# Kernel optimization log

Hardware: AMD Instinct MI355X
Metric: run time of the kernel (lower is better)

## Reference

```python
import jax, jax.numpy as jnp
import numpy as np
import jax.scipy.linalg as jsl

# ---- module constants (mirror __init__ buffers) ----
T0, T1, DT = 0.0, 1.0, 1e-3
DIM, NSTEPS, M, TQ, B = 8, 2048, 64, 1024, 1
DS = (T1 - T0) / NSTEPS
STEPS = jnp.linspace(T0, T1, NSTEPS + 1)            # [S+1]
ZPTS = jnp.linspace(T0 + DT * 5.5, T1 - DT * 5.5, M)  # inducing points [M]
SQRT_DS = float(np.sqrt(DS))
SQRT_DT = float(np.sqrt(DT))


def _hurst(t, y0, W1, b1, W2, b2, Wc1, bc1, Wc2, bc2, dw, cw):
    # compute_hurst: sigmoid(driving_action(t)*dw + condition_net(y0)*cw)
    tc_in = t.reshape(-1, 1)                                             # [N,1]
    feat = jnp.concatenate([jnp.sin(tc_in), jnp.cos(tc_in), tc_in], -1)  # [N,3]
    tc = jax.nn.sigmoid(jnp.tanh(feat @ W1.T + b1) @ W2.T + b2)          # [N,dim]
    pc = jax.nn.sigmoid(jnp.tanh(y0 @ Wc1.T + bc1) @ Wc2.T + bc2)        # [1,dim]
    return jax.nn.sigmoid(tc * dw + pc * cw)                             # [N,dim]


def _safe_pow(x, a):
    # x**a for x>=0, with well-defined (zero) gradient at x==0
    mask = x > 0
    xs = jnp.where(mask, x, 1.0)
    return jnp.where(mask, xs ** a, 0.0)


def _compute_weight(t, y0, params, eps=1e-12):
    # compute_weight (Muniandy et al. weight); returns [S, N, dim]
    h = _hurst(t, y0, *params)[None]                              # [1,N,dim]
    d0 = jax.nn.relu(t[None, :] - STEPS[:-1, None])[..., None]    # [S,N,1]
    d1 = jax.nn.relu(t[None, :] - STEPS[1:, None])[..., None]     # [S,N,1]
    w = jnp.sqrt(_safe_pow(d0, 2.0 * h) - _safe_pow(d1, 2.0 * h) + eps)
    w = w / jnp.sqrt(2.0 * h * DS)
    return w / jnp.exp(jax.lax.lgamma(h + 0.5))


def _increment_weight(t, y0, params):
    # increment_weight: g_i / dt (finite difference of clamped weights)
    wa = jnp.maximum(_compute_weight(t, y0, params), 0.0)
    wb = jnp.maximum(_compute_weight(t + DT, y0, params), 0.0)
    return jnp.maximum((wb - wa) * SQRT_DS / DT, 0.0)             # [S,N,dim]


def _forward(t, y0, eps_z, W1, b1, W2, b2, Wc1, bc1, Wc2, bc2, dw, cw):
    params = (W1, b1, W2, b2, Wc1, bc1, Wc2, bc2, dw, cw)
    # --- precompute (inducing points) ---
    Kz = _increment_weight(ZPTS, y0, params)                # [S,M,dim]
    Kzz = jnp.einsum('smd,skd->dmk', Kz, Kz)                # [dim,M,M]
    Lz = jnp.linalg.cholesky(Kzz + 1e-6 * jnp.eye(M, dtype=Kzz.dtype))
    delta_Bz = jnp.einsum('dmk,dkb->dmb', Lz, eps_z)        # [dim,M,B]
    # --- forward (mean / sqrt(var)*sqrt(dt)) ---
    Kt = _increment_weight(t, y0, params)                   # [S,T,dim]
    Ktz = jnp.einsum('std,smd->dtm', Kt, Kz)                # [dim,T,M]
    alpha = jax.vmap(lambda L, b: jsl.cho_solve((L, True), b))(
        Lz, jnp.swapaxes(Ktz, -1, -2))                      # [dim,M,T]
    mean = jnp.einsum('dmt,dmb->dtb', alpha, delta_Bz)      # [dim,T,B]
    Ktt = jnp.einsum('std,sud->dtu', Kt, Kt)                # [dim,T,T]
    var = Ktt - jnp.einsum('dmt,dmu->dtu', alpha, alpha)    # [dim,T,T]
    std = jnp.sqrt(jnp.maximum(var, 1e-12)) * SQRT_DT
    return mean.reshape(-1, DIM), std.reshape(-1, DIM)


def setup_inputs() -> dict:
    key = jax.random.key(0)
    ks = jax.random.split(key, 12)
    return {
        't': jax.random.uniform(ks[0], (TQ,), jnp.float32, T0 + 0.05, T1 - 0.05),
        'y0': jax.random.normal(ks[1], (1, 1), jnp.float32),
        'eps_z': jax.random.normal(ks[2], (DIM, M, B), jnp.float32),
        'W1': jax.random.normal(ks[3], (10, 3), jnp.float32) * 0.3,
        'b1': jax.random.normal(ks[4], (10,), jnp.float32) * 0.1,
        'W2': jax.random.normal(ks[5], (DIM, 10), jnp.float32) * 0.3,
        'b2': jax.random.normal(ks[6], (DIM,), jnp.float32) * 0.1,
        'Wc1': jax.random.normal(ks[7], (10, 1), jnp.float32) * 0.3,
        'bc1': jax.random.normal(ks[8], (10,), jnp.float32) * 0.1,
        'Wc2': jax.random.normal(ks[9], (DIM, 10), jnp.float32) * 0.3,
        'bc2': jax.random.normal(ks[10], (DIM,), jnp.float32) * 0.1,
        'dw': jnp.array([0.5], jnp.float32),
        'cw': jnp.array([0.5], jnp.float32),
    }


def reference(t, y0, eps_z, W1, b1, W2, b2, Wc1, bc1, Wc2, bc2, dw, cw):
    return _forward(t, y0, eps_z, W1, b1, W2, b2, Wc1, bc1, Wc2, bc2, dw, cw)
```

## Files before the change

kernel.cpp:

```cpp
#include <hip/hip_runtime.h>
#include <cmath>

#define DIMN 8
#define SSTEPS 2048
#define MZ 64
#define TQN 1024
#define DS_F    4.8828125e-4f
#define DT_F    1.0e-3f
#define SCALE_F 22.09708691207961f
#define SQRTDT_F 0.031622776601683794f
#define LN2_F   0.6931471805599453f

typedef _Float16 f16x8 __attribute__((ext_vector_type(8)));
typedef float f32x4 __attribute__((ext_vector_type(4)));

__device__ __forceinline__ float sigmoidf_(float x) { return 1.f / (1.f + expf(-x)); }

__global__ void coef_kernel(const float* __restrict__ t_in, const float* __restrict__ y0,
                            const float* __restrict__ W1, const float* __restrict__ b1,
                            const float* __restrict__ W2, const float* __restrict__ b2,
                            const float* __restrict__ Wc1, const float* __restrict__ bc1,
                            const float* __restrict__ Wc2, const float* __restrict__ bc2,
                            const float* __restrict__ dw, const float* __restrict__ cw,
                            float4* __restrict__ coef_t, float4* __restrict__ coef_z,
                            float* __restrict__ times_z)
{
    int gid = blockIdx.x * blockDim.x + threadIdx.x;
    if (gid >= TQN + MZ) return;
    bool isz = gid >= TQN;
    float tv;
    if (!isz) {
        tv = t_in[gid];
    } else {
        int j = gid - TQN;
        tv = 0.0055f + (float)j * (0.989f / 63.0f);
        times_z[j] = tv;
    }
    float y = y0[0];
    float hc[10];
    #pragma unroll
    for (int j = 0; j < 10; ++j) hc[j] = tanhf(y * Wc1[j] + bc1[j]);
    float pc[DIMN];
    #pragma unroll
    for (int d = 0; d < DIMN; ++d) {
        float s = bc2[d];
        #pragma unroll
        for (int j = 0; j < 10; ++j) s += hc[j] * Wc2[d * 10 + j];
        pc[d] = sigmoidf_(s);
    }
    float dww = dw[0], cww = cw[0];
    float4 outv[DIMN];
    for (int which = 0; which < 2; ++which) {
        float tt = (which == 0) ? tv : tv + DT_F;
        float st = sinf(tt), ct = cosf(tt);
        float hid[10];
        #pragma unroll
        for (int j = 0; j < 10; ++j)
            hid[j] = tanhf(st * W1[j * 3 + 0] + ct * W1[j * 3 + 1] + tt * W1[j * 3 + 2] + b1[j]);
        #pragma unroll
        for (int d = 0; d < DIMN; ++d) {
            float s = b2[d];
            #pragma unroll
            for (int j = 0; j < 10; ++j) s += hid[j] * W2[d * 10 + j];
            float tc = sigmoidf_(s);
            float h = sigmoidf_(tc * dww + pc[d] * cww);
            float e = 2.f * h;
            float c = rsqrtf(e * DS_F) / tgammaf(h + 0.5f);
            if (which == 0) { outv[d].x = e; outv[d].y = c; }
            else            { outv[d].z = e; outv[d].w = c; }
        }
    }
    float4* dst = isz ? (coef_z + (size_t)(gid - TQN) * DIMN) : (coef_t + (size_t)gid * DIMN);
    #pragma unroll
    for (int d = 0; d < DIMN; ++d) dst[d] = outv[d];
}

__device__ __forceinline__ void side_weights(float tt, float e, float c, int sbase,
                                             float (&w)[8])
{
    float xprev = tt - (float)sbase * DS_F;
    float pa = 0.f;
    if (xprev > 0.f) pa = __builtin_amdgcn_exp2f(e * __builtin_amdgcn_logf(xprev));
    #pragma unroll
    for (int k = 1; k <= 8; ++k) {
        float xk = tt - (float)(sbase + k) * DS_F;
        float D, pan;
        if (xk > 0.f) {
            float om = xk * __builtin_amdgcn_rcpf(xprev);
            float y2 = e * __builtin_amdgcn_logf(om);
            float wl = y2 * LN2_F;
            float em = wl * (1.f + wl * (0.5f + wl * (0.16666667f + wl * (0.041666668f + wl * 0.008333334f))));
            float g = -em;
            if (wl < -0.3f) g = 1.f - __builtin_amdgcn_exp2f(y2);
            D = pa * g;
            pan = pa - D;
        } else {
            D = pa;
            pan = 0.f;
        }
        w[k - 1] = __builtin_amdgcn_sqrtf(D + 1e-12f) * c;
        pa = pan;
        xprev = xk;
    }
}

__device__ __forceinline__ unsigned pack_hl(float v)
{
    _Float16 h = (_Float16)v;
    _Float16 l = (_Float16)(v - (float)h);
    unsigned short hu = __builtin_bit_cast(unsigned short, h);
    unsigned short lu = __builtin_bit_cast(unsigned short, l);
    return (unsigned)hu | ((unsigned)lu << 16);
}

__global__ __launch_bounds__(256) void kmat_t_kernel(const float* __restrict__ times,
                                                     const float4* __restrict__ coef,
                                                     _Float16* __restrict__ KThi,
                                                     _Float16* __restrict__ KTlo)
{
    int tid = threadIdx.x;
    int txx = tid & 31, sidx = tid >> 5;
    int t = blockIdx.x * 32 + txx;
    int sbase = blockIdx.y * 64 + sidx * 8;
    int d = blockIdx.z;
    __shared__ unsigned shhl[32][65];
    float tq = times[t];
    float4 cf = coef[(size_t)t * DIMN + d];
    float wa[8], wb[8];
    side_weights(tq,        cf.x, cf.y, sbase, wa);
    side_weights(tq + DT_F, cf.z, cf.w, sbase, wb);
    #pragma unroll
    for (int k = 0; k < 8; ++k) {
        float v = fmaxf(wb[k] - wa[k], 0.f) * SCALE_F;
        shhl[txx][sidx * 8 + k] = pack_hl(v);
    }
    __syncthreads();
    int tl = tid >> 3, sc = tid & 7;
    unsigned dwv[8];
    #pragma unroll
    for (int j = 0; j < 8; ++j) dwv[j] = shhl[tl][sc * 8 + j];
    uint4 hv, lv;
    hv.x = __builtin_amdgcn_perm(dwv[1], dwv[0], 0x05040100u);
    hv.y = __builtin_amdgcn_perm(dwv[3], dwv[2], 0x05040100u);
    hv.z = __builtin_amdgcn_perm(dwv[5], dwv[4], 0x05040100u);
    hv.w = __builtin_amdgcn_perm(dwv[7], dwv[6], 0x05040100u);
    lv.x = __builtin_amdgcn_perm(dwv[1], dwv[0], 0x07060302u);
    lv.y = __builtin_amdgcn_perm(dwv[3], dwv[2], 0x07060302u);
    lv.z = __builtin_amdgcn_perm(dwv[5], dwv[4], 0x07060302u);
    lv.w = __builtin_amdgcn_perm(dwv[7], dwv[6], 0x07060302u);
    size_t o = ((size_t)(d * 1024) + blockIdx.x * 32 + tl) * 2048 + blockIdx.y * 64 + sc * 8;
    *(uint4*)&KThi[o] = hv;
    *(uint4*)&KTlo[o] = lv;
}

__global__ __launch_bounds__(256) void kmat_z_kernel(const float* __restrict__ times,
                                                     const float4* __restrict__ coef,
                                                     float* __restrict__ Kz,
                                                     _Float16* __restrict__ KzThi,
                                                     _Float16* __restrict__ KzTlo)
{
    int tid = threadIdx.x;
    int txx = tid & 31, sidx = tid >> 5;
    int m = blockIdx.x * 32 + txx;
    int sbase = blockIdx.y * 64 + sidx * 8;
    int d = blockIdx.z;
    __shared__ unsigned shhl[32][65];
    float tq = times[m];
    float4 cf = coef[(size_t)m * DIMN + d];
    float wa[8], wb[8];
    side_weights(tq,        cf.x, cf.y, sbase, wa);
    side_weights(tq + DT_F, cf.z, cf.w, sbase, wb);
    #pragma unroll
    for (int k = 0; k < 8; ++k) {
        float v = fmaxf(wb[k] - wa[k], 0.f) * SCALE_F;
        Kz[((size_t)d * SSTEPS + sbase + k) * 64 + m] = v;
        shhl[txx][sidx * 8 + k] = pack_hl(v);
    }
    __syncthreads();
    int tl = tid >> 3, sc = tid & 7;
    unsigned dwv[8];
    #pragma unroll
    for (int j = 0; j < 8; ++j) dwv[j] = shhl[tl][sc * 8 + j];
    uint4 hv, lv;
    hv.x = __builtin_amdgcn_perm(dwv[1], dwv[0], 0x05040100u);
    hv.y = __builtin_amdgcn_perm(dwv[3], dwv[2], 0x05040100u);
    hv.z = __builtin_amdgcn_perm(dwv[5], dwv[4], 0x05040100u);
    hv.w = __builtin_amdgcn_perm(dwv[7], dwv[6], 0x05040100u);
    lv.x = __builtin_amdgcn_perm(dwv[1], dwv[0], 0x07060302u);
    lv.y = __builtin_amdgcn_perm(dwv[3], dwv[2], 0x07060302u);
    lv.z = __builtin_amdgcn_perm(dwv[5], dwv[4], 0x07060302u);
    lv.w = __builtin_amdgcn_perm(dwv[7], dwv[6], 0x07060302u);
    size_t o = ((size_t)(d * 64) + blockIdx.x * 32 + tl) * 2048 + blockIdx.y * 64 + sc * 8;
    *(uint4*)&KzThi[o] = hv;
    *(uint4*)&KzTlo[o] = lv;
}

__global__ __launch_bounds__(256) void kzz_partial_kernel(const float* __restrict__ Kz,
                                                          float* __restrict__ part)
{
    int kidx = blockIdx.x;
    int d = blockIdx.y;
    int tid = threadIdx.x, tx = tid & 15, ty = tid >> 4;
    __shared__ float As[32][64];
    float acc[4][4] = {};
    const float* base = Kz + ((size_t)d * SSTEPS + (size_t)kidx * 256) * 64;
    for (int c = 0; c < 8; ++c) {
        __syncthreads();
        #pragma unroll
        for (int l = 0; l < 2; ++l) {
            int idx = tid + l * 256;
            int r = idx >> 4, c4 = idx & 15;
            *(float4*)&As[r][c4 * 4] = *(const float4*)(base + (size_t)(c * 32 + r) * 64 + c4 * 4);
        }
        __syncthreads();
        #pragma unroll
        for (int k = 0; k < 32; ++k) {
            float av[4], bv[4];
            *(float4*)&av[0] = *(float4*)&As[k][ty * 4];
            *(float4*)&bv[0] = *(float4*)&As[k][tx * 4];
            #pragma unroll
            for (int i = 0; i < 4; ++i)
                #pragma unroll
                for (int j = 0; j < 4; ++j) acc[i][j] += av[i] * bv[j];
        }
    }
    float* dst = part + (size_t)(kidx * DIMN + d) * 4096;
    #pragma unroll
    for (int i = 0; i < 4; ++i)
        *(float4*)&dst[(size_t)(ty * 4 + i) * 64 + tx * 4] =
            make_float4(acc[i][0], acc[i][1], acc[i][2], acc[i][3]);
}

__global__ void reduce_kernel(const float* __restrict__ in, float* __restrict__ out,
                              int n, int parts)
{
    int i = blockIdx.x * 256 + threadIdx.x;
    if (i >= n) return;
    float s = 0.f;
    for (int p = 0; p < parts; ++p) s += in[(size_t)p * n + i];
    out[i] = s;
}

__global__ __launch_bounds__(64) void chol_kernel(const float* __restrict__ Kzz,
                                                  const float* __restrict__ eps_z,
                                                  float* __restrict__ Lz, float* __restrict__ dBz)
{
    int d = blockIdx.x, i = threadIdx.x;
    __shared__ float A[64][65];
    for (int r = 0; r < 64; ++r)
        A[r][i] = Kzz[(size_t)d * 4096 + (size_t)r * 64 + i] + ((r == i) ? 1e-6f : 0.f);
    __syncthreads();
    for (int j = 0; j < 64; ++j) {
        float s = 0.f;
        if (i >= j) {
            s = A[i][j];
            for (int k = 0; k < j; ++k) s -= A[i][k] * A[j][k];
        }
        __syncthreads();
        if (i == j) A[j][j] = sqrtf(fmaxf(s, 1e-30f));
        __syncthreads();
        if (i > j) A[i][j] = s / A[j][j];
        __syncthreads();
    }
    for (int r = 0; r < 64; ++r)
        Lz[(size_t)d * 4096 + (size_t)r * 64 + i] = (i <= r) ? A[r][i] : 0.f;
    float s = 0.f;
    for (int k = 0; k <= i; ++k) s += A[i][k] * eps_z[d * 64 + k];
    dBz[d * 64 + i] = s;
}

__global__ __launch_bounds__(256) void ktz_mfma_kernel(const _Float16* __restrict__ KThi,
                                                       const _Float16* __restrict__ KTlo,
                                                       const _Float16* __restrict__ KzThi,
                                                       const _Float16* __restrict__ KzTlo,
                                                       float* __restrict__ part)
{
    int tid = threadIdx.x;
    int wave = tid >> 6, lane = tid & 63;
    int n = lane & 15, q = lane >> 4;
    int t0 = blockIdx.x * 128;
    int split = blockIdx.y;
    int d = blockIdx.z;
    int wr = (wave >> 1) * 64, wc = (wave & 1) * 32;

    __shared__ _Float16 Ah[128][40], Al[128][40];
    __shared__ _Float16 Bh[64][40],  Bl[64][40];

    f32x4 acc[4][2];
    #pragma unroll
    for (int i = 0; i < 4; ++i)
        #pragma unroll
        for (int j = 0; j < 2; ++j) acc[i][j] = (f32x4)0.f;

    const _Float16* ah = KThi + ((size_t)(d * 1024 + t0)) * 2048;
    const _Float16* al = KTlo + ((size_t)(d * 1024 + t0)) * 2048;
    const _Float16* bh = KzThi + ((size_t)(d * 64)) * 2048;
    const _Float16* bl = KzTlo + ((size_t)(d * 64)) * 2048;

    int s0end = split * 512 + 512;
    for (int s0 = split * 512; s0 < s0end; s0 += 32) {
        __syncthreads();
        #pragma unroll
        for (int l = 0; l < 2; ++l) {
            int idx = tid + l * 256;
            int r = idx >> 2, p = idx & 3;
            *(float4*)&Ah[r][p * 8] = *(const float4*)(ah + (size_t)r * 2048 + s0 + p * 8);
            *(float4*)&Al[r][p * 8] = *(const float4*)(al + (size_t)r * 2048 + s0 + p * 8);
        }
        {
            int r = tid >> 2, p = tid & 3;
            *(float4*)&Bh[r][p * 8] = *(const float4*)(bh + (size_t)r * 2048 + s0 + p * 8);
            *(float4*)&Bl[r][p * 8] = *(const float4*)(bl + (size_t)r * 2048 + s0 + p * 8);
        }
        __syncthreads();
        f16x8 fAh[4], fAl[4], fBh[2], fBl[2];
        #pragma unroll
        for (int i = 0; i < 4; ++i) {
            fAh[i] = *(f16x8*)&Ah[wr + i * 16 + n][q * 8];
            fAl[i] = *(f16x8*)&Al[wr + i * 16 + n][q * 8];
        }
        #pragma unroll
        for (int j = 0; j < 2; ++j) {
            fBh[j] = *(f16x8*)&Bh[wc + j * 16 + n][q * 8];
            fBl[j] = *(f16x8*)&Bl[wc + j * 16 + n][q * 8];
        }
        #pragma unroll
        for (int i = 0; i < 4; ++i)
            #pragma unroll
            for (int j = 0; j < 2; ++j) {
                acc[i][j] = __builtin_amdgcn_mfma_f32_16x16x32_f16(fAh[i], fBh[j], acc[i][j], 0, 0, 0);
                acc[i][j] = __builtin_amdgcn_mfma_f32_16x16x32_f16(fAh[i], fBl[j], acc[i][j], 0, 0, 0);
                acc[i][j] = __builtin_amdgcn_mfma_f32_16x16x32_f16(fAl[i], fBh[j], acc[i][j], 0, 0, 0);
            }
    }
    float* dst = part + ((size_t)(split * DIMN + d)) * 1024 * 64;
    #pragma unroll
    for (int i = 0; i < 4; ++i)
        #pragma unroll
        for (int j = 0; j < 2; ++j)
            #pragma unroll
            for (int r = 0; r < 4; ++r) {
                int t = t0 + wr + i * 16 + q * 4 + r;
                dst[(size_t)t * 64 + wc + j * 16 + n] = acc[i][j][r];
            }
}

__global__ __launch_bounds__(64) void solve_kernel(const float* __restrict__ Lz,
                                                   const float* __restrict__ Ktz,
                                                   float* __restrict__ alpha)
{
    int d = blockIdx.y;
    int t = blockIdx.x * 64 + threadIdx.x;
    __shared__ float L[64][65];
    __shared__ float inv[64];
    for (int r = 0; r < 64; ++r)
        L[r][threadIdx.x] = Lz[(size_t)d * 4096 + (size_t)r * 64 + threadIdx.x];
    __syncthreads();
    inv[threadIdx.x] = 1.f / L[threadIdx.x][threadIdx.x];
    __syncthreads();
    float b[64];
    const float4* src = (const float4*)(Ktz + ((size_t)d * 1024 + t) * 64);
    #pragma unroll
    for (int qq = 0; qq < 16; ++qq) {
        float4 v = src[qq];
        b[4 * qq] = v.x; b[4 * qq + 1] = v.y; b[4 * qq + 2] = v.z; b[4 * qq + 3] = v.w;
    }
    #pragma unroll
    for (int j = 0; j < 64; ++j) {
        float s = b[j];
        #pragma unroll
        for (int k = 0; k < j; ++k) s -= L[j][k] * b[k];
        b[j] = s * inv[j];
    }
    #pragma unroll
    for (int j = 63; j >= 0; --j) {
        float s = b[j];
        #pragma unroll
        for (int k = j + 1; k < 64; ++k) s -= L[k][j] * b[k];
        b[j] = s * inv[j];
    }
    #pragma unroll
    for (int m = 0; m < 64; ++m)
        alpha[((size_t)d * 64 + m) * 1024 + t] = b[m];
}

__global__ __launch_bounds__(256) void asplit_kernel(const float* __restrict__ alpha,
                                                     _Float16* __restrict__ aPhi,
                                                     _Float16* __restrict__ aPlo,
                                                     _Float16* __restrict__ aNhi,
                                                     _Float16* __restrict__ aNlo)
{
    int d = blockIdx.y, t0 = blockIdx.x * 64, tid = threadIdx.x;
    __shared__ float tile[64][68];
    #pragma unroll
    for (int l = 0; l < 4; ++l) {
        int idx = tid + l * 256;
        int r = idx >> 4, c4 = idx & 15;
        *(float4*)&tile[r][c4 * 4] =
            *(const float4*)(alpha + ((size_t)(d * 64 + r)) * 1024 + t0 + c4 * 4);
    }
    __syncthreads();
    int tl = tid & 63, sq = tid >> 6;
    union { _Float16 h[16]; float4 v[2]; } ph, pl, nh, nl;
    #pragma unroll
    for (int k = 0; k < 16; ++k) {
        float x = tile[sq * 16 + k][tl];
        _Float16 h = (_Float16)x;
        _Float16 lo = (_Float16)(x - (float)h);
        ph.h[k] = h;  pl.h[k] = lo;
        nh.h[k] = -h; nl.h[k] = -lo;
    }
    size_t o = ((size_t)(d * 1024 + t0 + tl)) * 64 + sq * 16;
    *(float4*)&aPhi[o] = ph.v[0]; *(float4*)&aPhi[o + 8] = ph.v[1];
    *(float4*)&aPlo[o] = pl.v[0]; *(float4*)&aPlo[o + 8] = pl.v[1];
    *(float4*)&aNhi[o] = nh.v[0]; *(float4*)&aNhi[o + 8] = nh.v[1];
    *(float4*)&aNlo[o] = nl.v[0]; *(float4*)&aNlo[o + 8] = nl.v[1];
}

__global__ void mean_kernel(const float* __restrict__ alpha, const float* __restrict__ dBz,
                            float* __restrict__ out0)
{
    int g = blockIdx.x * 256 + threadIdx.x;
    int d = g >> 10, t = g & 1023;
    float s = 0.f;
    for (int m = 0; m < 64; ++m) s += alpha[((size_t)d * 64 + m) * 1024 + t] * dBz[d * 64 + m];
    out0[g] = s;
}

__global__ __launch_bounds__(256) void var_mfma_kernel(const _Float16* __restrict__ KThi,
                                                       const _Float16* __restrict__ KTlo,
                                                       const _Float16* __restrict__ aPhi,
                                                       const _Float16* __restrict__ aPlo,
                                                       const _Float16* __restrict__ aNhi,
                                                       const _Float16* __restrict__ aNlo,
                                                       float* __restrict__ out1)
{
    int tid = threadIdx.x;
    int wave = tid >> 6, lane = tid & 63;
    int n = lane & 15, q = lane >> 4;
    int d = blockIdx.z;
    int t0 = blockIdx.x * 128, u0 = blockIdx.y * 128;
    int wr = (wave >> 1) * 64, wc = (wave & 1) * 64;

    __shared__ _Float16 Ah[128][40], Al[128][40], Bh[128][40], Bl[128][40];

    f32x4 acc[4][4];
    #pragma unroll
    for (int i = 0; i < 4; ++i)
        #pragma unroll
        for (int j = 0; j < 4; ++j) acc[i][j] = (f32x4)0.f;

    for (int ck = 0; ck < 66; ++ck) {
        const _Float16 *pAh, *pAl, *pBh, *pBl;
        size_t astr;
        if (ck < 64) {
            size_t ao = ((size_t)(d * 1024 + t0)) * 2048 + ck * 32;
            size_t bo = ((size_t)(d * 1024 + u0)) * 2048 + ck * 32;
            pAh = KThi + ao; pAl = KTlo + ao;
            pBh = KThi + bo; pBl = KTlo + bo;
            astr = 2048;
        } else {
            size_t ao = ((size_t)(d * 1024 + t0)) * 64 + (ck - 64) * 32;
            size_t bo = ((size_t)(d * 1024 + u0)) * 64 + (ck - 64) * 32;
            pAh = aPhi + ao; pAl = aPlo + ao;
            pBh = aNhi + bo; pBl = aNlo + bo;
            astr = 64;
        }
        __syncthreads();
        #pragma unroll
        for (int l = 0; l < 2; ++l) {
            int idx = tid + l * 256;
            int r = idx >> 2, p = idx & 3;
            size_t go = (size_t)r * astr + p * 8;
            *(float4*)&Ah[r][p * 8] = *(const float4*)(pAh + go);
            *(float4*)&Al[r][p * 8] = *(const float4*)(pAl + go);
            *(float4*)&Bh[r][p * 8] = *(const float4*)(pBh + go);
            *(float4*)&Bl[r][p * 8] = *(const float4*)(pBl + go);
        }
        __syncthreads();
        f16x8 fAh[4], fAl[4], fBh[4], fBl[4];
        #pragma unroll
        for (int i = 0; i < 4; ++i) {
            fAh[i] = *(f16x8*)&Ah[wr + i * 16 + n][q * 8];
            fAl[i] = *(f16x8*)&Al[wr + i * 16 + n][q * 8];
            fBh[i] = *(f16x8*)&Bh[wc + i * 16 + n][q * 8];
            fBl[i] = *(f16x8*)&Bl[wc + i * 16 + n][q * 8];
        }
        #pragma unroll
        for (int i = 0; i < 4; ++i)
            #pragma unroll
            for (int j = 0; j < 4; ++j) {
                acc[i][j] = __builtin_amdgcn_mfma_f32_16x16x32_f16(fAh[i], fBh[j], acc[i][j], 0, 0, 0);
                acc[i][j] = __builtin_amdgcn_mfma_f32_16x16x32_f16(fAh[i], fBl[j], acc[i][j], 0, 0, 0);
                acc[i][j] = __builtin_amdgcn_mfma_f32_16x16x32_f16(fAl[i], fBh[j], acc[i][j], 0, 0, 0);
            }
    }
    float* dst = out1 + ((size_t)d << 20);
    #pragma unroll
    for (int i = 0; i < 4; ++i)
        #pragma unroll
        for (int j = 0; j < 4; ++j)
            #pragma unroll
            for (int r = 0; r < 4; ++r) {
                int t = t0 + wr + i * 16 + q * 4 + r;
                int u = u0 + wc + j * 16 + n;
                float v = acc[i][j][r];
                dst[(size_t)t * 1024 + u] = sqrtf(fmaxf(v, 1e-12f)) * SQRTDT_F;
            }
}

extern "C" void kernel_launch(void* const* d_in, const int* in_sizes, int n_in,
                              void* d_out, int out_size, void* d_ws, size_t ws_size,
                              hipStream_t stream)
{
    const float* t_in  = (const float*)d_in[0];
    const float* y0    = (const float*)d_in[1];
    const float* eps_z = (const float*)d_in[2];
    const float* W1    = (const float*)d_in[3];
    const float* b1    = (const float*)d_in[4];
    const float* W2    = (const float*)d_in[5];
    const float* b2    = (const float*)d_in[6];
    const float* Wc1   = (const float*)d_in[7];
    const float* bc1   = (const float*)d_in[8];
    const float* Wc2   = (const float*)d_in[9];
    const float* bc2   = (const float*)d_in[10];
    const float* dw    = (const float*)d_in[11];
    const float* cw    = (const float*)d_in[12];

    float* ws = (float*)d_ws;
    size_t off = 0;
    auto carve = [&](size_t n) { float* p = ws + off; off += n; return p; };
    float* coef_t   = carve(32768);
    float* coef_z   = carve(2048);
    float* times_z  = carve(64);
    float* Kzz      = carve(32768);
    float* Lz       = carve(32768);
    float* dBz      = carve(512);
    float* Kz       = carve(1048576);
    _Float16* KThi  = (_Float16*)carve(8388608);
    _Float16* KTlo  = (_Float16*)carve(8388608);
    _Float16* KzThi = (_Float16*)carve(524288);
    _Float16* KzTlo = (_Float16*)carve(524288);
    float* Ktz      = carve(524288);
    float* alphaA   = carve(524288);
    float* part1    = carve(262144);
    float* part2    = carve(2097152);
    _Float16* aPhi  = (_Float16*)carve(262144);
    _Float16* aPlo  = (_Float16*)carve(262144);
    _Float16* aNhi  = (_Float16*)carve(262144);
    _Float16* aNlo  = (_Float16*)carve(262144);

    float* out0 = (float*)d_out;
    float* out1 = out0 + (size_t)DIMN * 1024;

    coef_kernel<<<9, 128, 0, stream>>>(t_in, y0, W1, b1, W2, b2, Wc1, bc1, Wc2, bc2, dw, cw,
                                       (float4*)coef_t, (float4*)coef_z, times_z);
    kmat_t_kernel<<<dim3(32, 32, 8), 256, 0, stream>>>(t_in, (const float4*)coef_t,
                                                       KThi, KTlo);
    kmat_z_kernel<<<dim3(2, 32, 8), 256, 0, stream>>>(times_z, (const float4*)coef_z,
                                                      Kz, KzThi, KzTlo);
    kzz_partial_kernel<<<dim3(8, 8), 256, 0, stream>>>(Kz, part1);
    reduce_kernel<<<128, 256, 0, stream>>>(part1, Kzz, 32768, 8);
    chol_kernel<<<8, 64, 0, stream>>>(Kzz, eps_z, Lz, dBz);
    ktz_mfma_kernel<<<dim3(8, 4, 8), 256, 0, stream>>>(KThi, KTlo, KzThi, KzTlo, part2);
    reduce_kernel<<<2048, 256, 0, stream>>>(part2, Ktz, 524288, 4);
    solve_kernel<<<dim3(16, 8), 64, 0, stream>>>(Lz, Ktz, alphaA);
    asplit_kernel<<<dim3(16, 8), 256, 0, stream>>>(alphaA, aPhi, aPlo, aNhi, aNlo);
    mean_kernel<<<32, 256, 0, stream>>>(alphaA, dBz, out0);
    var_mfma_kernel<<<dim3(8, 8, 8), 256, 0, stream>>>(KThi, KTlo, aPhi, aPlo, aNhi, aNlo, out1);
}
```

Before: 420.8 us.

## Fuse split-K reduce, asplit and mean into solve; remap grids and staging order

The triangular-solve kernel now sums the four split-K partials itself, computes the mean output, and writes the fp16 hi/lo positive and negative alpha splits directly. This removes the separate reduce, asplit and mean kernels along with their intermediate Ktz and alpha buffers. The grid order is also changed so the dim index is fastest-varying, and the shared-memory staging index mapping is permuted so each wavefront's global loads are grouped differently. The cost is that the solve kernel, with only 128 blocks of 64 threads, now does strided 4-way partial reads and scattered fp16 stores per thread.

```diff
diff --git a/kernel.cpp b/kernel.cpp
--- a/kernel.cpp
+++ b/kernel.cpp
@@ -15,6 +15,12 @@
 typedef float f32x4 __attribute__((ext_vector_type(4)));
 
 __device__ __forceinline__ float sigmoidf_(float x) { return 1.f / (1.f + expf(-x)); }
+
+__device__ __forceinline__ void stage_idx(int idx, int& r, int& p)
+{
+    r = (idx & 7) | ((idx >> 5) << 3);
+    p = (idx >> 3) & 3;
+}
 
 __global__ void coef_kernel(const float* __restrict__ t_in, const float* __restrict__ y0,
                             const float* __restrict__ W1, const float* __restrict__ b1,
@@ -278,9 +284,9 @@
     int tid = threadIdx.x;
     int wave = tid >> 6, lane = tid & 63;
     int n = lane & 15, q = lane >> 4;
-    int t0 = blockIdx.x * 128;
-    int split = blockIdx.y;
-    int d = blockIdx.z;
+    int d = blockIdx.x;
+    int t0 = blockIdx.y * 128;
+    int split = blockIdx.z;
     int wr = (wave >> 1) * 64, wc = (wave & 1) * 32;
 
     __shared__ _Float16 Ah[128][40], Al[128][40];
@@ -302,13 +308,12 @@
         __syncthreads();
         #pragma unroll
         for (int l = 0; l < 2; ++l) {
-            int idx = tid + l * 256;
-            int r = idx >> 2, p = idx & 3;
+            int r, p; stage_idx(tid + l * 256, r, p);
             *(float4*)&Ah[r][p * 8] = *(const float4*)(ah + (size_t)r * 2048 + s0 + p * 8);
             *(float4*)&Al[r][p * 8] = *(const float4*)(al + (size_t)r * 2048 + s0 + p * 8);
         }
         {
-            int r = tid >> 2, p = tid & 3;
+            int r, p; stage_idx(tid, r, p);
             *(float4*)&Bh[r][p * 8] = *(const float4*)(bh + (size_t)r * 2048 + s0 + p * 8);
             *(float4*)&Bl[r][p * 8] = *(const float4*)(bl + (size_t)r * 2048 + s0 + p * 8);
         }
@@ -346,24 +351,36 @@
 }
 
 __global__ __launch_bounds__(64) void solve_kernel(const float* __restrict__ Lz,
-                                                   const float* __restrict__ Ktz,
-                                                   float* __restrict__ alpha)
+                                                   const float* __restrict__ part2,
+                                                   const float* __restrict__ dBz,
+                                                   _Float16* __restrict__ aPhi,
+                                                   _Float16* __restrict__ aPlo,
+                                                   _Float16* __restrict__ aNhi,
+                                                   _Float16* __restrict__ aNlo,
+                                                   float* __restrict__ out0)
 {
     int d = blockIdx.y;
     int t = blockIdx.x * 64 + threadIdx.x;
     __shared__ float L[64][65];
     __shared__ float inv[64];
+    __shared__ float dB[64];
     for (int r = 0; r < 64; ++r)
         L[r][threadIdx.x] = Lz[(size_t)d * 4096 + (size_t)r * 64 + threadIdx.x];
+    dB[threadIdx.x] = dBz[d * 64 + threadIdx.x];
     __syncthreads();
     inv[threadIdx.x] = 1.f / L[threadIdx.x][threadIdx.x];
     __syncthreads();
     float b[64];
-    const float4* src = (const float4*)(Ktz + ((size_t)d * 1024 + t) * 64);
     #pragma unroll
     for (int qq = 0; qq < 16; ++qq) {
-        float4 v = src[qq];
-        b[4 * qq] = v.x; b[4 * qq + 1] = v.y; b[4 * qq + 2] = v.z; b[4 * qq + 3] = v.w;
+        float4 a0 = *(const float4*)(part2 + ((size_t)(0 * 8 + d) * 1024 + t) * 64 + qq * 4);
+        float4 a1 = *(const float4*)(part2 + ((size_t)(1 * 8 + d) * 1024 + t) * 64 + qq * 4);
+        float4 a2 = *(const float4*)(part2 + ((size_t)(2 * 8 + d) * 1024 + t) * 64 + qq * 4);
+        float4 a3 = *(const float4*)(part2 + ((size_t)(3 * 8 + d) * 1024 + t) * 64 + qq * 4);
+        b[4 * qq]     = a0.x + a1.x + a2.x + a3.x;
+        b[4 * qq + 1] = a0.y + a1.y + a2.y + a3.y;
+        b[4 * qq + 2] = a0.z + a1.z + a2.z + a3.z;
+        b[4 * qq + 3] = a0.w + a1.w + a2.w + a3.w;
     }
     #pragma unroll
     for (int j = 0; j < 64; ++j) {
@@ -379,52 +396,27 @@
         for (int k = j + 1; k < 64; ++k) s -= L[k][j] * b[k];
         b[j] = s * inv[j];
     }
-    #pragma unroll
-    for (int m = 0; m < 64; ++m)
-        alpha[((size_t)d * 64 + m) * 1024 + t] = b[m];
-}
-
-__global__ __launch_bounds__(256) void asplit_kernel(const float* __restrict__ alpha,
-                                                     _Float16* __restrict__ aPhi,
-                                                     _Float16* __restrict__ aPlo,
-                                                     _Float16* __restrict__ aNhi,
-                                                     _Float16* __restrict__ aNlo)
-{
-    int d = blockIdx.y, t0 = blockIdx.x * 64, tid = threadIdx.x;
-    __shared__ float tile[64][68];
-    #pragma unroll
-    for (int l = 0; l < 4; ++l) {
-        int idx = tid + l * 256;
-        int r = idx >> 4, c4 = idx & 15;
-        *(float4*)&tile[r][c4 * 4] =
-            *(const float4*)(alpha + ((size_t)(d * 64 + r)) * 1024 + t0 + c4 * 4);
-    }
-    __syncthreads();
-    int tl = tid & 63, sq = tid >> 6;
-    union { _Float16 h[16]; float4 v[2]; } ph, pl, nh, nl;
-    #pragma unroll
-    for (int k = 0; k < 16; ++k) {
-        float x = tile[sq * 16 + k][tl];
-        _Float16 h = (_Float16)x;
-        _Float16 lo = (_Float16)(x - (float)h);
-        ph.h[k] = h;  pl.h[k] = lo;
-        nh.h[k] = -h; nl.h[k] = -lo;
-    }
-    size_t o = ((size_t)(d * 1024 + t0 + tl)) * 64 + sq * 16;
-    *(float4*)&aPhi[o] = ph.v[0]; *(float4*)&aPhi[o + 8] = ph.v[1];
-    *(float4*)&aPlo[o] = pl.v[0]; *(float4*)&aPlo[o + 8] = pl.v[1];
-    *(float4*)&aNhi[o] = nh.v[0]; *(float4*)&aNhi[o + 8] = nh.v[1];
-    *(float4*)&aNlo[o] = nl.v[0]; *(float4*)&aNlo[o + 8] = nl.v[1];
-}
-
-__global__ void mean_kernel(const float* __restrict__ alpha, const float* __restrict__ dBz,
-                            float* __restrict__ out0)
-{
-    int g = blockIdx.x * 256 + threadIdx.x;
-    int d = g >> 10, t = g & 1023;
-    float s = 0.f;
-    for (int m = 0; m < 64; ++m) s += alpha[((size_t)d * 64 + m) * 1024 + t] * dBz[d * 64 + m];
-    out0[g] = s;
+    float mn = 0.f;
+    #pragma unroll
+    for (int m = 0; m < 64; ++m) mn += b[m] * dB[m];
+    out0[d * 1024 + t] = mn;
+    size_t o = ((size_t)(d * 1024 + t)) * 64;
+    #pragma unroll
+    for (int g = 0; g < 8; ++g) {
+        union { _Float16 h[8]; float4 v; } ph, pl, nh, nl;
+        #pragma unroll
+        for (int k = 0; k < 8; ++k) {
+            float x = b[g * 8 + k];
+            _Float16 h = (_Float16)x;
+            _Float16 lo = (_Float16)(x - (float)h);
+            ph.h[k] = h;  pl.h[k] = lo;
+            nh.h[k] = -h; nl.h[k] = -lo;
+        }
+        *(float4*)&aPhi[o + g * 8] = ph.v;
+        *(float4*)&aPlo[o + g * 8] = pl.v;
+        *(float4*)&aNhi[o + g * 8] = nh.v;
+        *(float4*)&aNlo[o + g * 8] = nl.v;
+    }
 }
 
 __global__ __launch_bounds__(256) void var_mfma_kernel(const _Float16* __restrict__ KThi,
@@ -438,8 +430,8 @@
     int tid = threadIdx.x;
     int wave = tid >> 6, lane = tid & 63;
     int n = lane & 15, q = lane >> 4;
-    int d = blockIdx.z;
-    int t0 = blockIdx.x * 128, u0 = blockIdx.y * 128;
+    int d = blockIdx.x;
+    int t0 = blockIdx.y * 128, u0 = blockIdx.z * 128;
     int wr = (wave >> 1) * 64, wc = (wave & 1) * 64;
 
     __shared__ _Float16 Ah[128][40], Al[128][40], Bh[128][40], Bl[128][40];
@@ -469,8 +461,7 @@
         __syncthreads();
         #pragma unroll
         for (int l = 0; l < 2; ++l) {
-            int idx = tid + l * 256;
-            int r = idx >> 2, p = idx & 3;
+            int r, p; stage_idx(tid + l * 256, r, p);
             size_t go = (size_t)r * astr + p * 8;
             *(float4*)&Ah[r][p * 8] = *(const float4*)(pAh + go);
             *(float4*)&Al[r][p * 8] = *(const float4*)(pAl + go);
@@ -541,8 +532,6 @@
     _Float16* KTlo  = (_Float16*)carve(8388608);
     _Float16* KzThi = (_Float16*)carve(524288);
     _Float16* KzTlo = (_Float16*)carve(524288);
-    float* Ktz      = carve(524288);
-    float* alphaA   = carve(524288);
     float* part1    = carve(262144);
     float* part2    = carve(2097152);
     _Float16* aPhi  = (_Float16*)carve(262144);
@@ -562,10 +551,7 @@
     kzz_partial_kernel<<<dim3(8, 8), 256, 0, stream>>>(Kz, part1);
     reduce_kernel<<<128, 256, 0, stream>>>(part1, Kzz, 32768, 8);
     chol_kernel<<<8, 64, 0, stream>>>(Kzz, eps_z, Lz, dBz);
-    ktz_mfma_kernel<<<dim3(8, 4, 8), 256, 0, stream>>>(KThi, KTlo, KzThi, KzTlo, part2);
-    reduce_kernel<<<2048, 256, 0, stream>>>(part2, Ktz, 524288, 4);
-    solve_kernel<<<dim3(16, 8), 64, 0, stream>>>(Lz, Ktz, alphaA);
-    asplit_kernel<<<dim3(16, 8), 256, 0, stream>>>(alphaA, aPhi, aPlo, aNhi, aNlo);
-    mean_kernel<<<32, 256, 0, stream>>>(alphaA, dBz, out0);
+    ktz_mfma_kernel<<<dim3(8, 8, 4), 256, 0, stream>>>(KThi, KTlo, KzThi, KzTlo, part2);
+    solve_kernel<<<dim3(16, 8), 64, 0, stream>>>(Lz, part2, dBz, aPhi, aPlo, aNhi, aNlo, out0);
     var_mfma_kernel<<<dim3(8, 8, 8), 256, 0, stream>>>(KThi, KTlo, aPhi, aPlo, aNhi, aNlo, out1);
 }
```

Result: slower. 468.2 us (+11.3%).
